# Kernel tuning notes

Hardware: AMD Instinct MI355X
Metric: run time of the kernel (lower is better)

The kernel has to match this reference:

```python
import jax, jax.numpy as jnp
import numpy as np

UNITS = 512
D_DEC = 1024
D_ENC = 1024


def setup_inputs() -> dict:
    key = jax.random.key(0)
    ks = jax.random.split(key, 8)
    B, S = 32, 2048
    decoder_hidden = jax.random.normal(ks[0], (B, 1, D_DEC), dtype=jnp.float32)
    encoder_outputs = jax.random.normal(ks[1], (B, S, D_ENC), dtype=jnp.float32)
    # Dense layer params (glorot-ish scale)
    W1 = jax.random.normal(ks[2], (D_DEC, UNITS), dtype=jnp.float32) * (1.0 / np.sqrt(D_DEC))
    b1 = jnp.zeros((UNITS,), dtype=jnp.float32)
    W2 = jax.random.normal(ks[3], (D_ENC, UNITS), dtype=jnp.float32) * (1.0 / np.sqrt(D_ENC))
    b2 = jnp.zeros((UNITS,), dtype=jnp.float32)
    V = jax.random.normal(ks[4], (UNITS, 1), dtype=jnp.float32) * (1.0 / np.sqrt(UNITS))
    bv = jnp.zeros((1,), dtype=jnp.float32)
    return {
        "decoder_hidden": decoder_hidden,
        "encoder_outputs": encoder_outputs,
        "W1": W1, "b1": b1, "W2": W2, "b2": b2, "V": V, "bv": bv,
    }


def reference(decoder_hidden, encoder_outputs, W1, b1, W2, b2, V, bv):
    # query: [B, 1, units]
    query = jnp.einsum('bqd,du->bqu', decoder_hidden, W1) + b1
    # values: [B, S, units]
    values = jnp.einsum('bsd,du->bsu', encoder_outputs, W2) + b2
    # scores: [B, S, 1]
    scores = jnp.einsum('bsu,uo->bso', jnp.tanh(query + values), V) + bv
    # softmax over sequence axis (axis=1)
    attention_weights = jax.nn.softmax(scores, axis=1)
    # context: [B, d_enc]
    context_vector = jnp.sum(attention_weights * encoder_outputs, axis=1)
    return context_vector, attention_weights
```

## Files before the change

### kernel.cpp

```cpp
#include <hip/hip_runtime.h>
#include <hip/hip_bf16.h>
#include <hip/hip_fp16.h>

#define UNITS 512
#define D_DEC 1024
#define D_ENC 1024
#define BATCH 32
#define S_LEN 2048

typedef _Float16 f16x8 __attribute__((ext_vector_type(8)));
typedef float f32x4 __attribute__((ext_vector_type(4)));

__device__ inline float tanh_fast(float x) {
    float e = __expf(2.f * x);
    return 1.f - 2.f * __builtin_amdgcn_rcpf(e + 1.f);
}

__global__ __launch_bounds__(256) void k_prep(const float* __restrict__ W2,
                                              _Float16* __restrict__ W2h,
                                              const float* __restrict__ dec,
                                              const float* __restrict__ W1,
                                              const float* __restrict__ b1,
                                              float* __restrict__ query) {
    const int tid = threadIdx.x;
    if (blockIdx.x < 512) {
        __shared__ float tile[32][33];
        const int kb = (blockIdx.x & 31) * 32;
        const int nb = (blockIdx.x >> 5) * 32;
        const int tx = tid & 31;
        const int ty = tid >> 5;
        for (int i = 0; i < 32; i += 8)
            tile[ty + i][tx] = W2[(size_t)(kb + ty + i) * UNITS + nb + tx];
        __syncthreads();
        for (int i = 0; i < 32; i += 8)
            W2h[(size_t)(nb + ty + i) * D_DEC + kb + tx] = (_Float16)tile[tx][ty + i];
    } else {
        const int qb = blockIdx.x - 512;
        const int u  = (qb >> 2) * 32 + (tid & 31);
        const int b  = (qb & 3) * 8 + (tid >> 5);
        float acc = b1[u];
        const float* dp = dec + (size_t)b * D_DEC;
        const float* wp = W1 + u;
        for (int d = 0; d < D_DEC; ++d) acc += dp[d] * wp[(size_t)d * UNITS];
        query[(size_t)b * UNITS + u] = acc;
    }
}

#define BM 128
#define BKK 32
#define NSTEP (D_DEC / BKK)

__global__ __launch_bounds__(1024, 4) void k_fused(const float* __restrict__ enc,
                                                   const _Float16* __restrict__ W2h,
                                                   const float* __restrict__ query,
                                                   const float* __restrict__ b2,
                                                   const float* __restrict__ V,
                                                   float* __restrict__ scores,
                                                   float* __restrict__ chunk_m,
                                                   float* __restrict__ chunk_l,
                                                   float* __restrict__ part_ctx) {
    __shared__ __align__(16) _Float16 Ab[2][BM * BKK];
    __shared__ __align__(16) _Float16 Bb[2][UNITS * BKK];
    __shared__ float sc_part[8][BM];
    __shared__ float sc_e[BM];
    __shared__ float wred[4];

    const int tid  = threadIdx.x;
    const int lane = tid & 63;
    const int w    = tid >> 6;
    const int wr   = w >> 3;
    const int wc   = w & 7;
    const int g    = lane >> 4;
    const int r    = lane & 15;
    const int blk  = blockIdx.x;
    const int row0 = blk * BM;
    const int bat  = row0 >> 11;

    int offA[4], offB[4];
#pragma unroll
    for (int q = 0; q < 4; ++q) {
        const int rowa = wr * 64 + q * 16 + r;
        offA[q] = rowa * 64 + ((g * 16) ^ (((rowa >> 1) & 3) << 4));
    }
#pragma unroll
    for (int q = 0; q < 4; ++q) {
        const int rowb = wc * 64 + q * 16 + r;
        offB[q] = rowb * 64 + ((g * 16) ^ (((rowb >> 1) & 3) << 4));
    }

    const int arow = tid >> 3;
    const int ac4  = tid & 7;
    const float* ap = enc + (size_t)(row0 + arow) * D_ENC + ac4 * 4;
    const int a_wbyte = arow * 64 + ((ac4 * 8) ^ (((arow >> 1) & 3) << 4));

    const int bn0  = tid >> 2;
    const int bj   = tid & 3;
    const int kel0 = ((bj * 16) ^ (((bn0 >> 1) & 3) << 4)) >> 1;
    const _Float16* bsrc0 = W2h + (size_t)bn0 * D_DEC + kel0;
    const int bn1  = (1024 + tid) >> 2;
    const int kel1 = ((bj * 16) ^ (((bn1 >> 1) & 3) << 4)) >> 1;
    const _Float16* bsrc1 = W2h + (size_t)bn1 * D_DEC + kel1;
    const int bdst0 = tid * 16;
    const int bdst1 = (1024 + tid) * 16;

    f32x4 acc[4][4];
#pragma unroll
    for (int i = 0; i < 4; ++i)
#pragma unroll
        for (int j = 0; j < 4; ++j) acc[i][j] = (f32x4){0.f, 0.f, 0.f, 0.f};

    auto gldB = [&](int t, int buf) {
        char* base = (char*)&Bb[buf][0];
        __builtin_amdgcn_global_load_lds(
            (const __attribute__((address_space(1))) void*)(bsrc0 + t * BKK),
            (__attribute__((address_space(3))) void*)(base + bdst0), 16, 0, 0);
        __builtin_amdgcn_global_load_lds(
            (const __attribute__((address_space(1))) void*)(bsrc1 + t * BKK),
            (__attribute__((address_space(3))) void*)(base + bdst1), 16, 0, 0);
    };
    auto cvtA = [&](const float4& p, int buf) {
        _Float16 h[4] = {(_Float16)p.x, (_Float16)p.y, (_Float16)p.z, (_Float16)p.w};
        *reinterpret_cast<float2*>((char*)&Ab[buf][0] + a_wbyte) =
            *reinterpret_cast<float2*>(h);
    };

    {
        const float4 p0 = *reinterpret_cast<const float4*>(ap);
        gldB(0, 0);
        cvtA(p0, 0);
    }
    __syncthreads();

    for (int t = 0; t < NSTEP; ++t) {
        const int cur = t & 1;
        float4 pn;
        if (t + 1 < NSTEP) {
            pn = *reinterpret_cast<const float4*>(ap + (t + 1) * BKK);
            gldB(t + 1, cur ^ 1);
        }

        const char* Ac = (const char*)&Ab[cur][0];
        const char* Bc = (const char*)&Bb[cur][0];
        f16x8 af[4], bf[4];
#pragma unroll
        for (int q = 0; q < 4; ++q) af[q] = *reinterpret_cast<const f16x8*>(Ac + offA[q]);
#pragma unroll
        for (int q = 0; q < 4; ++q) bf[q] = *reinterpret_cast<const f16x8*>(Bc + offB[q]);
#pragma unroll
        for (int fr = 0; fr < 4; ++fr)
#pragma unroll
            for (int fc = 0; fc < 4; ++fc)
                acc[fr][fc] = __builtin_amdgcn_mfma_f32_16x16x32_f16(
                    af[fr], bf[fc], acc[fr][fc], 0, 0, 0);

        if (t + 1 < NSTEP) cvtA(pn, cur ^ 1);
        __syncthreads();
    }

    float qv[4], vv[4];
#pragma unroll
    for (int fc = 0; fc < 4; ++fc) {
        const int col = wc * 64 + fc * 16 + r;
        qv[fc] = query[(size_t)bat * UNITS + col] + b2[col];
        vv[fc] = V[col];
    }
    float ps[4][4];
#pragma unroll
    for (int fr = 0; fr < 4; ++fr)
#pragma unroll
        for (int i = 0; i < 4; ++i) ps[fr][i] = 0.f;
#pragma unroll
    for (int fc = 0; fc < 4; ++fc)
#pragma unroll
        for (int fr = 0; fr < 4; ++fr)
#pragma unroll
            for (int i = 0; i < 4; ++i)
                ps[fr][i] += tanh_fast(acc[fr][fc][i] + qv[fc]) * vv[fc];
#pragma unroll
    for (int off = 1; off < 16; off <<= 1)
#pragma unroll
        for (int fr = 0; fr < 4; ++fr)
#pragma unroll
            for (int i = 0; i < 4; ++i)
                ps[fr][i] += __shfl_xor(ps[fr][i], off, 64);
    if (r == 0)
#pragma unroll
        for (int fr = 0; fr < 4; ++fr)
#pragma unroll
            for (int i = 0; i < 4; ++i)
                sc_part[wc][wr * 64 + fr * 16 + g * 4 + i] = ps[fr][i];
    __syncthreads();

    float s_val = 0.f;
    if (tid < BM) {
#pragma unroll
        for (int ww = 0; ww < 8; ++ww) s_val += sc_part[ww][tid];
        scores[(size_t)row0 + tid] = s_val;
        float m = s_val;
#pragma unroll
        for (int off = 32; off; off >>= 1) m = fmaxf(m, __shfl_xor(m, off, 64));
        if ((tid & 63) == 0) wred[tid >> 6] = m;
    }
    __syncthreads();
    if (tid < BM) {
        const float M = fmaxf(wred[0], wred[1]);
        const float e = __expf(s_val - M);
        sc_e[tid] = e;
        float l = e;
#pragma unroll
        for (int off = 32; off; off >>= 1) l += __shfl_xor(l, off, 64);
        if ((tid & 63) == 0) wred[2 + (tid >> 6)] = l;
    }
    __syncthreads();
    if (tid == 0) {
        chunk_m[blk] = fmaxf(wred[0], wred[1]);
        chunk_l[blk] = wred[2] + wred[3];
    }

    {
        const int d = tid;
        float cx = 0.f;
        const float* ebase = enc + (size_t)row0 * D_ENC + d;
#pragma unroll 4
        for (int i = 0; i < BM; ++i)
            cx += sc_e[i] * ebase[(size_t)i * D_ENC];
        part_ctx[(size_t)blk * D_ENC + d] = cx;
    }
}

__global__ __launch_bounds__(256) void k_combine(const float* __restrict__ scores,
                                                 const float* __restrict__ chunk_m,
                                                 const float* __restrict__ chunk_l,
                                                 const float* __restrict__ part_ctx,
                                                 float* __restrict__ out_ctx,
                                                 float* __restrict__ out_w) {
    const int b = blockIdx.x;
    const int tid = threadIdx.x;
    __shared__ float fc[16];
    __shared__ float Msh, Lsh;
    if (tid < 16) {
        const float m = chunk_m[b * 16 + tid];
        float M = m;
#pragma unroll
        for (int off = 8; off; off >>= 1) M = fmaxf(M, __shfl_xor(M, off, 16));
        const float f = __expf(m - M);
        float lf = chunk_l[b * 16 + tid] * f;
#pragma unroll
        for (int off = 8; off; off >>= 1) lf += __shfl_xor(lf, off, 16);
        fc[tid] = f;
        if (tid == 0) { Msh = M; Lsh = lf; }
    }
    __syncthreads();
    const float M = Msh;
    const float invL = 1.f / Lsh;
#pragma unroll
    for (int j = 0; j < 8; ++j) {
        const int s = tid + j * 256;
        out_w[(size_t)b * S_LEN + s] = __expf(scores[(size_t)b * S_LEN + s] - M) * invL;
    }
#pragma unroll
    for (int j = 0; j < 4; ++j) {
        const int d = tid + j * 256;
        float sacc = 0.f;
        for (int c = 0; c < 16; ++c)
            sacc += part_ctx[(size_t)(b * 16 + c) * D_ENC + d] * fc[c];
        out_ctx[(size_t)b * D_ENC + d] = sacc * invL;
    }
}

extern "C" void kernel_launch(void* const* d_in, const int* in_sizes, int n_in,
                              void* d_out, int out_size, void* d_ws, size_t ws_size,
                              hipStream_t stream) {
    const float* dec = (const float*)d_in[0];
    const float* enc = (const float*)d_in[1];
    const float* W1  = (const float*)d_in[2];
    const float* b1  = (const float*)d_in[3];
    const float* W2  = (const float*)d_in[4];
    const float* b2  = (const float*)d_in[5];
    const float* V   = (const float*)d_in[6];

    float* out = (float*)d_out;
    float* out_ctx = out;
    float* out_w   = out + BATCH * D_ENC;

    char* ws = (char*)d_ws;
    _Float16* W2h  = (_Float16*)(ws);
    float* query   = (float*)(ws + (1 << 20));
    float* scores  = (float*)(ws + (1 << 20) + (1 << 16));
    float* chunk_m = (float*)(ws + (1 << 20) + (1 << 16) + (1 << 18));
    float* chunk_l = (float*)(ws + (1 << 20) + (1 << 16) + (1 << 18) + 4096);
    float* part_ctx = (float*)(ws + (1 << 20) + (1 << 16) + (1 << 18) + 8192);

    k_prep<<<576, 256, 0, stream>>>(W2, W2h, dec, W1, b1, query);
    k_fused<<<(BATCH * S_LEN) / BM, 1024, 0, stream>>>(enc, W2h, query, b2, V,
                                                       scores, chunk_m, chunk_l, part_ctx);
    k_combine<<<BATCH, 256, 0, stream>>>(scores, chunk_m, chunk_l, part_ctx,
                                         out_ctx, out_w);
}
```

Before: 181.5 us.

## Load encoder tile asynchronously to LDS as fp32 with triple-buffered pipeline

The encoder A tile is now fetched with global_load_lds straight into LDS as fp32, using an XOR swizzle. The fp16 conversion moves to fragment-read time, so the kernel no longer stages A through registers and converts before the store. The mainloop switches from double to triple buffering, with manual vmcnt/lgkmcnt waits and raw barriers so two stages of loads stay in flight. The cost is more LDS (fp32 A across three buffers, about 144KB in total), which may cap occupancy. It also doubles the LDS read traffic for A and adds conversion instructions in the inner loop.

```diff
diff --git a/kernel.cpp b/kernel.cpp
--- a/kernel.cpp
+++ b/kernel.cpp
@@ -49,6 +49,8 @@
 #define BM 128
 #define BKK 32
 #define NSTEP (D_DEC / BKK)
+#define ASZ (BM * BKK)
+#define BSZ (UNITS * BKK)
 
 __global__ __launch_bounds__(1024, 4) void k_fused(const float* __restrict__ enc,
                                                    const _Float16* __restrict__ W2h,
@@ -59,8 +61,8 @@
                                                    float* __restrict__ chunk_m,
                                                    float* __restrict__ chunk_l,
                                                    float* __restrict__ part_ctx) {
-    __shared__ __align__(16) _Float16 Ab[2][BM * BKK];
-    __shared__ __align__(16) _Float16 Bb[2][UNITS * BKK];
+    __shared__ __align__(16) float    Ab[3][ASZ];
+    __shared__ __align__(16) _Float16 Bb[3][BSZ];
     __shared__ float sc_part[8][BM];
     __shared__ float sc_e[BM];
     __shared__ float wred[4];
@@ -76,11 +78,13 @@
     const int row0 = blk * BM;
     const int bat  = row0 >> 11;
 
-    int offA[4], offB[4];
+    int offA0[4], offA1[4], offB[4];
 #pragma unroll
     for (int q = 0; q < 4; ++q) {
         const int rowa = wr * 64 + q * 16 + r;
-        offA[q] = rowa * 64 + ((g * 16) ^ (((rowa >> 1) & 3) << 4));
+        const int s    = (rowa & 7) << 4;
+        offA0[q] = rowa * 128 + ((g * 32) ^ s);
+        offA1[q] = rowa * 128 + ((g * 32 + 16) ^ s);
     }
 #pragma unroll
     for (int q = 0; q < 4; ++q) {
@@ -89,17 +93,18 @@
     }
 
     const int arow = tid >> 3;
-    const int ac4  = tid & 7;
-    const float* ap = enc + (size_t)(row0 + arow) * D_ENC + ac4 * 4;
-    const int a_wbyte = arow * 64 + ((ac4 * 8) ^ (((arow >> 1) & 3) << 4));
+    const int akb  = (tid & 7) * 16;
+    const float* asrc = enc + (size_t)(row0 + arow) * D_ENC
+                        + ((akb ^ ((arow & 7) << 4)) >> 2);
+    const int adst = tid * 16;
 
     const int bn0  = tid >> 2;
     const int bj   = tid & 3;
-    const int kel0 = ((bj * 16) ^ (((bn0 >> 1) & 3) << 4)) >> 1;
-    const _Float16* bsrc0 = W2h + (size_t)bn0 * D_DEC + kel0;
+    const _Float16* bsrc0 = W2h + (size_t)bn0 * D_DEC
+                            + (((bj * 16) ^ (((bn0 >> 1) & 3) << 4)) >> 1);
     const int bn1  = (1024 + tid) >> 2;
-    const int kel1 = ((bj * 16) ^ (((bn1 >> 1) & 3) << 4)) >> 1;
-    const _Float16* bsrc1 = W2h + (size_t)bn1 * D_DEC + kel1;
+    const _Float16* bsrc1 = W2h + (size_t)bn1 * D_DEC
+                            + (((bj * 16) ^ (((bn1 >> 1) & 3) << 4)) >> 1);
     const int bdst0 = tid * 16;
     const int bdst1 = (1024 + tid) * 16;
 
@@ -109,6 +114,12 @@
 #pragma unroll
         for (int j = 0; j < 4; ++j) acc[i][j] = (f32x4){0.f, 0.f, 0.f, 0.f};
 
+    auto gldA = [&](int t, int buf) {
+        __builtin_amdgcn_global_load_lds(
+            (const __attribute__((address_space(1))) void*)(asrc + t * BKK),
+            (__attribute__((address_space(3))) void*)((char*)&Ab[buf][0] + adst),
+            16, 0, 0);
+    };
     auto gldB = [&](int t, int buf) {
         char* base = (char*)&Bb[buf][0];
         __builtin_amdgcn_global_load_lds(
@@ -118,44 +129,52 @@
             (const __attribute__((address_space(1))) void*)(bsrc1 + t * BKK),
             (__attribute__((address_space(3))) void*)(base + bdst1), 16, 0, 0);
     };
-    auto cvtA = [&](const float4& p, int buf) {
-        _Float16 h[4] = {(_Float16)p.x, (_Float16)p.y, (_Float16)p.z, (_Float16)p.w};
-        *reinterpret_cast<float2*>((char*)&Ab[buf][0] + a_wbyte) =
-            *reinterpret_cast<float2*>(h);
-    };
-
-    {
-        const float4 p0 = *reinterpret_cast<const float4*>(ap);
-        gldB(0, 0);
-        cvtA(p0, 0);
-    }
-    __syncthreads();
-
-    for (int t = 0; t < NSTEP; ++t) {
-        const int cur = t & 1;
-        float4 pn;
-        if (t + 1 < NSTEP) {
-            pn = *reinterpret_cast<const float4*>(ap + (t + 1) * BKK);
-            gldB(t + 1, cur ^ 1);
+    auto compute = [&](int buf) {
+        const char* Ac = (const char*)&Ab[buf][0];
+        const char* Bc = (const char*)&Bb[buf][0];
+        f16x8 af[4], bf[4];
+#pragma unroll
+        for (int q = 0; q < 4; ++q) {
+            const f32x4 lo = *reinterpret_cast<const f32x4*>(Ac + offA0[q]);
+            const f32x4 hi = *reinterpret_cast<const f32x4*>(Ac + offA1[q]);
+            af[q] = (f16x8){(_Float16)lo.x, (_Float16)lo.y, (_Float16)lo.z, (_Float16)lo.w,
+                            (_Float16)hi.x, (_Float16)hi.y, (_Float16)hi.z, (_Float16)hi.w};
         }
-
-        const char* Ac = (const char*)&Ab[cur][0];
-        const char* Bc = (const char*)&Bb[cur][0];
-        f16x8 af[4], bf[4];
-#pragma unroll
-        for (int q = 0; q < 4; ++q) af[q] = *reinterpret_cast<const f16x8*>(Ac + offA[q]);
-#pragma unroll
-        for (int q = 0; q < 4; ++q) bf[q] = *reinterpret_cast<const f16x8*>(Bc + offB[q]);
+#pragma unroll
+        for (int q = 0; q < 4; ++q)
+            bf[q] = *reinterpret_cast<const f16x8*>(Bc + offB[q]);
 #pragma unroll
         for (int fr = 0; fr < 4; ++fr)
 #pragma unroll
             for (int fc = 0; fc < 4; ++fc)
                 acc[fr][fc] = __builtin_amdgcn_mfma_f32_16x16x32_f16(
                     af[fr], bf[fc], acc[fr][fc], 0, 0, 0);
-
-        if (t + 1 < NSTEP) cvtA(pn, cur ^ 1);
-        __syncthreads();
-    }
+    };
+
+    gldA(0, 0); gldB(0, 0);
+    gldA(1, 1); gldB(1, 1);
+    asm volatile("s_waitcnt vmcnt(3)" ::: "memory");
+    __builtin_amdgcn_s_barrier();
+
+#define STEP_FULL(T, BUF, NB) do {                                  \
+        gldA((T) + 2, NB); gldB((T) + 2, NB);                       \
+        compute(BUF);                                               \
+        asm volatile("s_waitcnt vmcnt(3)" ::: "memory");            \
+        asm volatile("s_waitcnt lgkmcnt(0)" ::: "memory");          \
+        __builtin_amdgcn_s_barrier();                               \
+    } while (0)
+
+    for (int t3 = 0; t3 < 30; t3 += 3) {
+        STEP_FULL(t3 + 0, 0, 2);
+        STEP_FULL(t3 + 1, 1, 0);
+        STEP_FULL(t3 + 2, 2, 1);
+    }
+#undef STEP_FULL
+    compute(0);
+    asm volatile("s_waitcnt vmcnt(0)" ::: "memory");
+    asm volatile("s_waitcnt lgkmcnt(0)" ::: "memory");
+    __builtin_amdgcn_s_barrier();
+    compute(1);
 
     float qv[4], vv[4];
 #pragma unroll
```

After: 177.5 us, median of 2. 1.02x faster.
